# Performance work log

Measured on AMD Instinct MI355X. Metric: run time of the kernel, lower is better.

The kernel has to match this reference:

```python
import jax, jax.numpy as jnp
import numpy as np

B = 512
AUDIO_H, VIDEO_H, TEXT_H = 64, 64, 128
POST_DIM = 128
FUSION_DIM = (TEXT_H + 1) * (VIDEO_H + 1) * (AUDIO_H + 1)  # 129*65*65 = 545025


def setup_inputs() -> dict:
    key = jax.random.key(0)
    ks = jax.random.split(key, 9)
    s1 = 1.0 / np.sqrt(FUSION_DIM)
    s2 = 1.0 / np.sqrt(POST_DIM)
    return {
        "audio_h": jax.random.normal(ks[0], (B, AUDIO_H), jnp.float32),
        "video_h": jax.random.normal(ks[1], (B, VIDEO_H), jnp.float32),
        "text_h": jax.random.normal(ks[2], (B, TEXT_H), jnp.float32),
        "W1": jax.random.uniform(ks[3], (FUSION_DIM, POST_DIM), jnp.float32, -s1, s1),
        "b1": jax.random.uniform(ks[4], (POST_DIM,), jnp.float32, -s1, s1),
        "W2": jax.random.uniform(ks[5], (POST_DIM, POST_DIM), jnp.float32, -s2, s2),
        "b2": jax.random.uniform(ks[6], (POST_DIM,), jnp.float32, -s2, s2),
        "W3": jax.random.uniform(ks[7], (POST_DIM, 1), jnp.float32, -s2, s2),
        "b3": jax.random.uniform(ks[8], (1,), jnp.float32, -s2, s2),
    }


def reference(audio_h, video_h, text_h, W1, b1, W2, b2, W3, b3):
    b = audio_h.shape[0]
    ones = jnp.ones((b, 1), audio_h.dtype)
    a1 = jnp.concatenate([ones, audio_h], axis=1)  # [B, A+1]
    v1 = jnp.concatenate([ones, video_h], axis=1)  # [B, V+1]
    t1 = jnp.concatenate([ones, text_h], axis=1)   # [B, T+1]
    # trilinear outer product: [B, T+1, V+1, A+1]
    fusion = jnp.einsum('bi,bj,bk->bijk', t1, v1, a1)
    flat = fusion.reshape(b, -1)  # [B, FUSION_DIM]
    # post-fusion MLP (dropout probs = 0 -> identity at inference)
    y1 = jax.nn.relu(flat @ W1 + b1)
    y2 = jax.nn.relu(y1 @ W2 + b2)
    y3 = jax.nn.sigmoid(y2 @ W3 + b3)
    # affine map to [-3, 3]: output_range=6, output_shift=-3
    return y3 * 6.0 - 3.0
```

## Files before the change

### kernel.cpp

```cpp
#include <hip/hip_runtime.h>
#include <hip/hip_bf16.h>
#include <math.h>

#define POST 128
#define NI 129
#define NJK 4225
#define NTOT 16512
#define KBLKS 134
#define MBLKS 32
#define KHALF 67
#define PANEL_CLAMP 2163184u

typedef __attribute__((ext_vector_type(8))) short bf16x8;
typedef __attribute__((ext_vector_type(4))) float f32x4;
typedef __attribute__((ext_vector_type(4))) unsigned int u32x4;

__device__ __forceinline__ unsigned short f2bf(float f){
    unsigned u = __builtin_bit_cast(unsigned, f);
    unsigned r = (u + 0x7FFFu + ((u >> 16) & 1u)) >> 16;
    return (unsigned short)r;
}
__device__ __forceinline__ unsigned pack2(float a, float b){
    return (unsigned)f2bf(a) | ((unsigned)f2bf(b) << 16);
}
__device__ __forceinline__ unsigned cvtpk(float lo, float hi){
    unsigned r;
    asm("v_cvt_pk_bf16_f32 %0, %1, %2" : "=v"(r) : "v"(lo), "v"(hi));
    return r;
}

__device__ __forceinline__ void gload16(const void* g, void* l){
    __builtin_amdgcn_global_load_lds(
        (const __attribute__((address_space(1))) unsigned int*)g,
        (__attribute__((address_space(3))) unsigned int*)l, 16, 0, 0);
}

__global__ void build_af(const float* __restrict__ audio,
                         const float* __restrict__ video,
                         uint4* __restrict__ af)
{
    int gid = blockIdx.x * 256 + threadIdx.x;
    if (gid >= KBLKS * MBLKS * 64) return;
    int lane = gid & 63;
    int mblk = (gid >> 6) & 31;
    int kblk = gid >> 11;
    int m  = mblk * 16 + (lane & 15);
    int k0 = kblk * 32 + (lane >> 4) * 8;
    float vals[8];
#pragma unroll
    for (int j = 0; j < 8; ++j){
        int k = k0 + j;
        float p = 0.f;
        if (k < NJK){
            int jj = k / 65;
            int kk = k - jj * 65;
            float a = (kk == 0) ? 1.f : audio[m * 64 + kk - 1];
            float v = (jj == 0) ? 1.f : video[m * 64 + jj - 1];
            p = a * v;
        }
        vals[j] = p;
    }
    uint4 o;
    o.x = pack2(vals[0], vals[1]);
    o.y = pack2(vals[2], vals[3]);
    o.z = pack2(vals[4], vals[5]);
    o.w = pack2(vals[6], vals[7]);
    af[gid] = o;
}

__global__ __launch_bounds__(256, 4) void fusion_gemm(
    const float* __restrict__ W1,
    const uint4* __restrict__ af,
    float* __restrict__ Z0,
    float* __restrict__ Z1)
{
    __shared__ __align__(16) char lds[32768];

    int orig = blockIdx.x;
    int xcd  = orig & 7;
    int w    = xcd * 129 + (orig >> 3);
    int nt  = w >> 3;
    int sub = w & 7;
    int mt  = sub & 3;
    int kb  = sub >> 2;

    int t    = threadIdx.x;
    int lane = t & 63;
    int wv   = t >> 6;
    int wm   = wv >> 1, wn = wv & 1;

    f32x4 acc[4][4] = {};

    const char* wpanel = (const char*)(W1 + (size_t)nt * (NJK * 128));

    int n_c = t & 127;
    int kg  = t >> 7;

    int ks0 = kb * KHALF;

#define STAGE(ks_)                                                              \
    do {                                                                        \
        _Pragma("unroll")                                                       \
        for (int i_ = 0; i_ < 4; ++i_){                                         \
            int c_ = wv * 4 + i_;                                               \
            unsigned bo_ = (unsigned)(ks_) * 16384u                             \
                         + (unsigned)c_ * 1024u + (unsigned)lane * 16u;         \
            if (bo_ > PANEL_CLAMP) bo_ = PANEL_CLAMP;            \
            gload16(wpanel + bo_, lds + c_ * 1024);                             \
        }                                                                       \
    } while (0)

    STAGE(ks0);

    for (int it = 0; it < KHALF; ++it){
        int ks = ks0 + it;
        int p  = it & 1;

        const uint4* abase = af + ((size_t)ks * 32 + mt * 8 + wm * 4) * 64 + lane;
        uint4 vA0 = abase[0];
        uint4 vA1 = abase[64];
        uint4 vA2 = abase[128];
        uint4 vA3 = abase[192];
        __builtin_amdgcn_sched_barrier(0);

        asm volatile("s_waitcnt vmcnt(4)" ::: "memory");
        __builtin_amdgcn_sched_barrier(0);
        __builtin_amdgcn_s_barrier();

        {
            char* fragp = lds + 16384 + p * 8192;
            float v[16];
#pragma unroll
            for (int j = 0; j < 16; ++j)
                v[j] = *(const float*)(lds + (kg * 16 + j) * 512 + n_c * 4);
            u32x4 u0, u1;
            u0.x = cvtpk(v[0],  v[1]);  u0.y = cvtpk(v[2],  v[3]);
            u0.z = cvtpk(v[4],  v[5]);  u0.w = cvtpk(v[6],  v[7]);
            u1.x = cvtpk(v[8],  v[9]);  u1.y = cvtpk(v[10], v[11]);
            u1.z = cvtpk(v[12], v[13]); u1.w = cvtpk(v[14], v[15]);
            int swz = ((n_c >> 1) & 3) << 4;
            *(u32x4*)(fragp + ((n_c * 64 + kg * 32     ) ^ swz)) = u0;
            *(u32x4*)(fragp + ((n_c * 64 + kg * 32 + 16) ^ swz)) = u1;
        }
        asm volatile("s_waitcnt lgkmcnt(0)" ::: "memory");
        __builtin_amdgcn_sched_barrier(0);
        __builtin_amdgcn_s_barrier();

        if (it + 1 < KHALF)
            STAGE(ks + 1);
        __builtin_amdgcn_sched_barrier(0);

        {
            const char* fragp = lds + 16384 + p * 8192;
            bf16x8 b[4];
#pragma unroll
            for (int g = 0; g < 4; ++g){
                int n = wn * 64 + g * 16 + (lane & 15);
                int byte = (n * 64 + (lane >> 4) * 16) ^ (((n >> 1) & 3) << 4);
                b[g] = *(const bf16x8*)(fragp + byte);
            }
            bf16x8 a0 = __builtin_bit_cast(bf16x8, vA0);
            bf16x8 a1 = __builtin_bit_cast(bf16x8, vA1);
            bf16x8 a2 = __builtin_bit_cast(bf16x8, vA2);
            bf16x8 a3 = __builtin_bit_cast(bf16x8, vA3);
#pragma unroll
            for (int g = 0; g < 4; ++g){
                acc[0][g] = __builtin_amdgcn_mfma_f32_16x16x32_bf16(a0, b[g], acc[0][g], 0, 0, 0);
                acc[1][g] = __builtin_amdgcn_mfma_f32_16x16x32_bf16(a1, b[g], acc[1][g], 0, 0, 0);
                acc[2][g] = __builtin_amdgcn_mfma_f32_16x16x32_bf16(a2, b[g], acc[2][g], 0, 0, 0);
                acc[3][g] = __builtin_amdgcn_mfma_f32_16x16x32_bf16(a3, b[g], acc[3][g], 0, 0, 0);
            }
        }
    }

    float* Zp = kb ? Z1 : Z0;
    int row0 = mt * 128 + wm * 64 + (lane >> 4) * 4;
    int col0 = nt * 128 + wn * 64 + (lane & 15);
#pragma unroll
    for (int f = 0; f < 4; ++f)
#pragma unroll
        for (int g = 0; g < 4; ++g)
#pragma unroll
            for (int r = 0; r < 4; ++r)
                Zp[(size_t)(row0 + f * 16 + r) * NTOT + col0 + g * 16] = acc[f][g][r];
}

__global__ void tail_mlp(const float* __restrict__ Z0,
                         const float* __restrict__ Z1,
                         const float* __restrict__ text,
                         const float* __restrict__ b1,
                         const float* __restrict__ W2,
                         const float* __restrict__ b2,
                         const float* __restrict__ W3,
                         const float* __restrict__ b3,
                         float* __restrict__ out)
{
    int b   = blockIdx.x;
    int tid = threadIdx.x;
    __shared__ float t1s[NI];
    __shared__ float y1s[POST];
    __shared__ float red[2];

    t1s[tid + 1] = text[b * 128 + tid];
    if (tid == 0) t1s[0] = 1.f;
    __syncthreads();

    const float* z0 = Z0 + (size_t)b * NTOT;
    const float* z1 = Z1 + (size_t)b * NTOT;
    float acc = 0.f;
    for (int i = 0; i < NI; ++i)
        acc = fmaf(t1s[i], z0[i * 128 + tid] + z1[i * 128 + tid], acc);
    acc += b1[tid];
    float y1 = fmaxf(acc, 0.f);
    y1s[tid] = y1;
    __syncthreads();

    float a2 = b2[tid];
    for (int q = 0; q < 128; ++q)
        a2 = fmaf(y1s[q], W2[q * 128 + tid], a2);
    float y2 = fmaxf(a2, 0.f);

    float part = y2 * W3[tid];
#pragma unroll
    for (int off = 32; off > 0; off >>= 1)
        part += __shfl_down(part, off);
    if ((tid & 63) == 0) red[tid >> 6] = part;
    __syncthreads();
    if (tid == 0){
        float z = red[0] + red[1] + b3[0];
        out[b] = 6.f / (1.f + expf(-z)) - 3.f;
    }
}

extern "C" void kernel_launch(void* const* d_in, const int* in_sizes, int n_in,
                              void* d_out, int out_size, void* d_ws, size_t ws_size,
                              hipStream_t stream)
{
    const float* audio = (const float*)d_in[0];
    const float* video = (const float*)d_in[1];
    const float* text  = (const float*)d_in[2];
    const float* W1    = (const float*)d_in[3];
    const float* b1    = (const float*)d_in[4];
    const float* W2    = (const float*)d_in[5];
    const float* b2    = (const float*)d_in[6];
    const float* W3    = (const float*)d_in[7];
    const float* b3    = (const float*)d_in[8];
    float* out = (float*)d_out;

    char* ws = (char*)d_ws;
    uint4* af = (uint4*)ws;
    float* Z0 = (float*)(ws + (8u  << 20));
    float* Z1 = (float*)(ws + (48u << 20));

    int af_granules = KBLKS * MBLKS * 64;
    build_af<<<(af_granules + 255) / 256, 256, 0, stream>>>(audio, video, af);
    fusion_gemm<<<1032, 256, 0, stream>>>(W1, af, Z0, Z1);
    tail_mlp<<<512, 128, 0, stream>>>(Z0, Z1, text, b1, W2, b2, W3, b3, out);
}
```

Before: 190.8 us.

## Give each GEMM block all 512 rows with four-way split-K to read W1 once

The fusion GEMM is reorganised so each 512-thread block covers all 512 batch rows and half of a 128-column N tile. K is split four ways instead of two, so each W1 element is fetched and converted to bf16 by only one block, rather than once per M tile. The next W1 stage is now prefetched before the barrier and the fp32-to-bf16 conversion work is spread over 8 waves. In exchange there are four fp32 partial Z buffers, which doubles the partial-sum write and read traffic in the tail kernel. It also needs a larger workspace.

Measured after the change: 188.6 us. About the same (-1.1%).

```diff
diff --git a/kernel.cpp b/kernel.cpp
--- a/kernel.cpp
+++ b/kernel.cpp
@@ -8,12 +8,12 @@
 #define NTOT 16512
 #define KBLKS 134
 #define MBLKS 32
-#define KHALF 67
+#define ZSTRIDE 8454144
 #define PANEL_CLAMP 2163184u
 
 typedef __attribute__((ext_vector_type(8))) short bf16x8;
 typedef __attribute__((ext_vector_type(4))) float f32x4;
-typedef __attribute__((ext_vector_type(4))) unsigned int u32x4;
+typedef __attribute__((ext_vector_type(2))) unsigned int u32x2;
 
 __device__ __forceinline__ unsigned short f2bf(float f){
     unsigned u = __builtin_bit_cast(unsigned, f);
@@ -68,101 +68,100 @@
     af[gid] = o;
 }
 
-__global__ __launch_bounds__(256, 4) void fusion_gemm(
+__global__ __launch_bounds__(512, 4) void fusion_gemm(
     const float* __restrict__ W1,
     const uint4* __restrict__ af,
-    float* __restrict__ Z0,
-    float* __restrict__ Z1)
-{
-    __shared__ __align__(16) char lds[32768];
+    float* __restrict__ Zbase)
+{
+    __shared__ __align__(16) char lds[20480];
 
     int orig = blockIdx.x;
     int xcd  = orig & 7;
     int w    = xcd * 129 + (orig >> 3);
     int nt  = w >> 3;
     int sub = w & 7;
-    int mt  = sub & 3;
-    int kb  = sub >> 2;
+    int nh  = sub & 1;
+    int kq  = sub >> 1;
+    int k0 = (kq < 2) ? kq * 34 : 68 + (kq - 2) * 33;
+    int NK = (kq < 2) ? 34 : 33;
 
     int t    = threadIdx.x;
     int lane = t & 63;
     int wv   = t >> 6;
-    int wm   = wv >> 1, wn = wv & 1;
 
     f32x4 acc[4][4] = {};
 
     const char* wpanel = (const char*)(W1 + (size_t)nt * (NJK * 128));
-
-    int n_c = t & 127;
-    int kg  = t >> 7;
-
-    int ks0 = kb * KHALF;
-
-#define STAGE(ks_)                                                              \
+    unsigned nhoff = (unsigned)nh * 256u;
+
+    int n_c = t & 63;
+
+    uint4 vA[4];
+
+#define STAGE(kb_, pb_)                                                         \
     do {                                                                        \
-        _Pragma("unroll")                                                       \
-        for (int i_ = 0; i_ < 4; ++i_){                                         \
-            int c_ = wv * 4 + i_;                                               \
-            unsigned bo_ = (unsigned)(ks_) * 16384u                             \
-                         + (unsigned)c_ * 1024u + (unsigned)lane * 16u;         \
-            if (bo_ > PANEL_CLAMP) bo_ = PANEL_CLAMP;            \
-            gload16(wpanel + bo_, lds + c_ * 1024);                             \
-        }                                                                       \
+        unsigned bo_ = (unsigned)(kb_) * 16384u                                 \
+                     + (unsigned)(wv * 4 + (lane >> 4)) * 512u                  \
+                     + nhoff + (unsigned)(lane & 15) * 16u;                     \
+        if (bo_ > PANEL_CLAMP) bo_ = PANEL_CLAMP;     \
+        gload16(wpanel + bo_, lds + (pb_) * 8192 + wv * 1024);                  \
     } while (0)
 
-    STAGE(ks0);
-
-    for (int it = 0; it < KHALF; ++it){
-        int ks = ks0 + it;
-        int p  = it & 1;
-
-        const uint4* abase = af + ((size_t)ks * 32 + mt * 8 + wm * 4) * 64 + lane;
-        uint4 vA0 = abase[0];
-        uint4 vA1 = abase[64];
-        uint4 vA2 = abase[128];
-        uint4 vA3 = abase[192];
-        __builtin_amdgcn_sched_barrier(0);
-
-        asm volatile("s_waitcnt vmcnt(4)" ::: "memory");
+    STAGE(k0, 0);
+
+    for (int it = 0; it < NK; ++it){
+        int kblk = k0 + it;
+        int p    = it & 1;
+
+        const uint4* ab = af + ((size_t)kblk * 32 + wv * 4) * 64 + lane;
+        vA[0] = ab[0];
+        vA[1] = ab[64];
+        vA[2] = ab[128];
+        vA[3] = ab[192];
+        __builtin_amdgcn_sched_barrier(0);
+
+        if (it + 1 < NK)
+            STAGE(kblk + 1, p ^ 1);
+        __builtin_amdgcn_sched_barrier(0);
+
+        if (it + 1 < NK){
+            asm volatile("s_waitcnt vmcnt(5)" ::: "memory");
+        } else {
+            asm volatile("s_waitcnt vmcnt(4)" ::: "memory");
+        }
         __builtin_amdgcn_sched_barrier(0);
         __builtin_amdgcn_s_barrier();
 
         {
-            char* fragp = lds + 16384 + p * 8192;
-            float v[16];
-#pragma unroll
-            for (int j = 0; j < 16; ++j)
-                v[j] = *(const float*)(lds + (kg * 16 + j) * 512 + n_c * 4);
-            u32x4 u0, u1;
-            u0.x = cvtpk(v[0],  v[1]);  u0.y = cvtpk(v[2],  v[3]);
-            u0.z = cvtpk(v[4],  v[5]);  u0.w = cvtpk(v[6],  v[7]);
-            u1.x = cvtpk(v[8],  v[9]);  u1.y = cvtpk(v[10], v[11]);
-            u1.z = cvtpk(v[12], v[13]); u1.w = cvtpk(v[14], v[15]);
-            int swz = ((n_c >> 1) & 3) << 4;
-            *(u32x4*)(fragp + ((n_c * 64 + kg * 32     ) ^ swz)) = u0;
-            *(u32x4*)(fragp + ((n_c * 64 + kg * 32 + 16) ^ swz)) = u1;
+            const char* rawp = lds + p * 8192;
+            char* fragp      = lds + 16384;
+            float v0 = *(const float*)(rawp + (wv * 4 + 0) * 256 + n_c * 4);
+            float v1 = *(const float*)(rawp + (wv * 4 + 1) * 256 + n_c * 4);
+            float v2 = *(const float*)(rawp + (wv * 4 + 2) * 256 + n_c * 4);
+            float v3 = *(const float*)(rawp + (wv * 4 + 3) * 256 + n_c * 4);
+            u32x2 uu;
+            uu.x = cvtpk(v0, v1);
+            uu.y = cvtpk(v2, v3);
+            int byte = (n_c * 64 + wv * 8) ^ (((n_c >> 1) & 3) << 4);
+            *(u32x2*)(fragp + byte) = uu;
         }
         asm volatile("s_waitcnt lgkmcnt(0)" ::: "memory");
         __builtin_amdgcn_sched_barrier(0);
         __builtin_amdgcn_s_barrier();
 
-        if (it + 1 < KHALF)
-            STAGE(ks + 1);
-        __builtin_amdgcn_sched_barrier(0);
-
         {
-            const char* fragp = lds + 16384 + p * 8192;
+            const char* fragp = lds + 16384;
             bf16x8 b[4];
 #pragma unroll
             for (int g = 0; g < 4; ++g){
-                int n = wn * 64 + g * 16 + (lane & 15);
+                int n = g * 16 + (lane & 15);
                 int byte = (n * 64 + (lane >> 4) * 16) ^ (((n >> 1) & 3) << 4);
                 b[g] = *(const bf16x8*)(fragp + byte);
             }
-            bf16x8 a0 = __builtin_bit_cast(bf16x8, vA0);
-            bf16x8 a1 = __builtin_bit_cast(bf16x8, vA1);
-            bf16x8 a2 = __builtin_bit_cast(bf16x8, vA2);
-            bf16x8 a3 = __builtin_bit_cast(bf16x8, vA3);
+            bf16x8 a0 = __builtin_bit_cast(bf16x8, vA[0]);
+            bf16x8 a1 = __builtin_bit_cast(bf16x8, vA[1]);
+            bf16x8 a2 = __builtin_bit_cast(bf16x8, vA[2]);
+            bf16x8 a3 = __builtin_bit_cast(bf16x8, vA[3]);
 #pragma unroll
             for (int g = 0; g < 4; ++g){
                 acc[0][g] = __builtin_amdgcn_mfma_f32_16x16x32_bf16(a0, b[g], acc[0][g], 0, 0, 0);
@@ -173,9 +172,9 @@
         }
     }
 
-    float* Zp = kb ? Z1 : Z0;
-    int row0 = mt * 128 + wm * 64 + (lane >> 4) * 4;
-    int col0 = nt * 128 + wn * 64 + (lane & 15);
+    float* Zp = Zbase + (size_t)kq * ZSTRIDE;
+    int row0 = wv * 64 + (lane >> 4) * 4;
+    int col0 = nt * 128 + nh * 64 + (lane & 15);
 #pragma unroll
     for (int f = 0; f < 4; ++f)
 #pragma unroll
@@ -185,8 +184,7 @@
                 Zp[(size_t)(row0 + f * 16 + r) * NTOT + col0 + g * 16] = acc[f][g][r];
 }
 
-__global__ void tail_mlp(const float* __restrict__ Z0,
-                         const float* __restrict__ Z1,
+__global__ void tail_mlp(const float* __restrict__ Zbase,
                          const float* __restrict__ text,
                          const float* __restrict__ b1,
                          const float* __restrict__ W2,
@@ -205,11 +203,16 @@
     if (tid == 0) t1s[0] = 1.f;
     __syncthreads();
 
-    const float* z0 = Z0 + (size_t)b * NTOT;
-    const float* z1 = Z1 + (size_t)b * NTOT;
+    const float* z0 = Zbase + (size_t)b * NTOT;
+    const float* z1 = z0 + (size_t)ZSTRIDE;
+    const float* z2 = z0 + (size_t)2 * ZSTRIDE;
+    const float* z3 = z0 + (size_t)3 * ZSTRIDE;
     float acc = 0.f;
-    for (int i = 0; i < NI; ++i)
-        acc = fmaf(t1s[i], z0[i * 128 + tid] + z1[i * 128 + tid], acc);
+    for (int i = 0; i < NI; ++i){
+        int idx = i * 128 + tid;
+        float zv = z0[idx] + z1[idx] + z2[idx] + z3[idx];
+        acc = fmaf(t1s[i], zv, acc);
+    }
     acc += b1[tid];
     float y1 = fmaxf(acc, 0.f);
     y1s[tid] = y1;
@@ -248,12 +251,11 @@
     float* out = (float*)d_out;
 
     char* ws = (char*)d_ws;
-    uint4* af = (uint4*)ws;
-    float* Z0 = (float*)(ws + (8u  << 20));
-    float* Z1 = (float*)(ws + (48u << 20));
+    uint4* af    = (uint4*)ws;
+    float* Zbase = (float*)(ws + (8u << 20));
 
     int af_granules = KBLKS * MBLKS * 64;
     build_af<<<(af_granules + 255) / 256, 256, 0, stream>>>(audio, video, af);
-    fusion_gemm<<<1032, 256, 0, stream>>>(W1, af, Z0, Z1);
-    tail_mlp<<<512, 128, 0, stream>>>(Z0, Z1, text, b1, W2, b2, W3, b3, out);
-}
+    fusion_gemm<<<1032, 512, 0, stream>>>(W1, af, Zbase);
+    tail_mlp<<<512, 128, 0, stream>>>(Zbase, text, b1, W2, b2, W3, b3, out);
+}
```
